# Kernel tuning notes

Measured on AMD Instinct MI355X. Metric: run time of the kernel, lower is better.

Reference implementation:

```python
import jax, jax.numpy as jnp
import numpy as np

B, S, D, H, E, TOPK = 8, 1024, 512, 2048, 8, 2


def setup_inputs() -> dict:
    key = jax.random.key(0)
    ks = jax.random.split(key, 7)
    scale = 0.02
    return {
        "x": jax.random.normal(ks[0], (B, S, D), jnp.float32),
        "gate_w": jax.random.normal(ks[1], (D, E), jnp.float32) * scale,
        "gate_b": jnp.zeros((E,), jnp.float32),
        "w1": jax.random.normal(ks[2], (E, D, H), jnp.float32) * scale,
        "b1": jnp.zeros((E, H), jnp.float32),
        "w2": jax.random.normal(ks[3], (E, H, D), jnp.float32) * scale,
        "b2": jnp.zeros((E, D), jnp.float32),
    }


def reference(x, gate_w, gate_b, w1, b1, w2, b2):
    # ---- MoE transformer MLP (fastmoe FMoETransformerMLP, NaiveGate) ----
    xt = x.reshape(-1, D)                       # [T, D], T = B*S tokens
    logits = xt @ gate_w + gate_b               # [T, E]
    top_val, top_idx = jax.lax.top_k(logits, TOPK)  # [T, k]
    score = jax.nn.softmax(top_val, axis=-1)    # softmax over the k selected logits

    y = jnp.zeros_like(xt)
    # Loop over the small fixed expert set; each token's combine weight for
    # expert e is the sum of its top-k scores routed to e (0 if not selected).
    for e in range(E):
        w_tok = jnp.sum(score * (top_idx == e), axis=-1)        # [T]
        h = jax.nn.gelu(xt @ w1[e] + b1[e], approximate=False)  # [T, H]
        y = y + w_tok[:, None] * (h @ w2[e] + b2[e])            # [T, D]

    y = y.reshape(B, S, D)
    # Outer model: log_softmax over seq of channel-summed features
    return jax.nn.log_softmax(jnp.sum(y, axis=2), axis=1)       # [B, S]
```

## Files before the change

kernel.cpp:

```cpp
#include <hip/hip_runtime.h>
#include <hip/hip_bf16.h>
#include <math.h>

#define T_TOK 8192
#define DIM   512
#define NEXP  8
#define HID   2048
#define NBAT  8
#define SEQ   1024

typedef short  short8 __attribute__((ext_vector_type(8)));
typedef float  f32x4  __attribute__((ext_vector_type(4)));

__device__ __forceinline__ unsigned short f2bf(float f) {
    union { float f; unsigned int u; } v; v.f = f;
    unsigned int u = v.u;
    unsigned int r = u + 0x7FFFu + ((u >> 16) & 1u);
    return (unsigned short)(r >> 16);
}

__device__ __forceinline__ float gelu_f(float v) {
    float v2 = v * v;
    float w = v * (-2.302344f - 0.102955f * v2);
    return v / (1.f + __builtin_amdgcn_exp2f(w));
}

__global__ void prep_k(const float* __restrict__ w1, unsigned short* __restrict__ w1t,
                       const float* __restrict__ w2, const float* __restrict__ b2,
                       float* __restrict__ w2sum, float* __restrict__ b2sum,
                       int* __restrict__ counts) {
    int bid = blockIdx.x;
    int tid = threadIdx.x;
    int wave = tid >> 6, lane = tid & 63;
    if (bid < 2048) {
        __shared__ unsigned short tile[64][65];
        int e = bid >> 8, r = bid & 255;
        int d0 = (r & 7) * 64, h0 = (r >> 3) * 64;
        const float* src = w1 + (size_t)e * DIM * HID;
        #pragma unroll
        for (int pass = 0; pass < 4; ++pass) {
            int dr = pass * 16 + (tid >> 4);
            int hc = (tid & 15) * 4;
            float4 v = *(const float4*)(src + (size_t)(d0 + dr) * HID + h0 + hc);
            tile[hc + 0][dr] = f2bf(v.x);
            tile[hc + 1][dr] = f2bf(v.y);
            tile[hc + 2][dr] = f2bf(v.z);
            tile[hc + 3][dr] = f2bf(v.w);
        }
        __syncthreads();
        unsigned short* dst = w1t + (size_t)e * HID * DIM;
        #pragma unroll
        for (int pass = 0; pass < 4; ++pass) {
            int hr = pass * 16 + (tid >> 4);
            int dc = (tid & 15) * 4;
            ushort4 o;
            o.x = tile[hr][dc];     o.y = tile[hr][dc + 1];
            o.z = tile[hr][dc + 2]; o.w = tile[hr][dc + 3];
            *(ushort4*)(dst + (size_t)(h0 + hr) * DIM + d0 + dc) = o;
        }
    } else if (bid < 2048 + 4096) {
        int row = (bid - 2048) * 4 + wave;
        const float* p = w2 + (size_t)row * DIM;
        float4 a = *(const float4*)(p + lane * 4);
        float4 b = *(const float4*)(p + 256 + lane * 4);
        float s = a.x + a.y + a.z + a.w + b.x + b.y + b.z + b.w;
        #pragma unroll
        for (int off = 32; off >= 1; off >>= 1) s += __shfl_xor(s, off);
        if (lane == 0) w2sum[row] = s;
    } else {
        if (tid < 8) counts[tid] = 0;
        for (int r = wave; r < NEXP; r += 4) {
            const float* p = b2 + (size_t)r * DIM;
            float s = 0.f;
            for (int i = lane; i < DIM; i += 64) s += p[i];
            #pragma unroll
            for (int off = 32; off >= 1; off >>= 1) s += __shfl_xor(s, off);
            if (lane == 0) b2sum[r] = s;
        }
    }
}

__global__ void gate2_k(const float* __restrict__ x, const float* __restrict__ gw,
                        const float* __restrict__ gb, const float* __restrict__ b2sum,
                        unsigned short* __restrict__ xb,
                        int* __restrict__ eidx, float* __restrict__ esc0,
                        float* __restrict__ esc1, float* __restrict__ s_partial) {
    int wave = threadIdx.x >> 6, lane = threadIdx.x & 63;
    int t = blockIdx.x * 4 + wave;
    const float* xp = x + (size_t)t * DIM;
    unsigned short* xbp = xb + (size_t)t * DIM;
    float acc[8] = {0, 0, 0, 0, 0, 0, 0, 0};
    #pragma unroll
    for (int it = 0; it < 8; ++it) {
        int d = it * 64 + lane;
        float xv = xp[d];
        xbp[d] = f2bf(xv);
        float4 g0 = *(const float4*)(gw + d * 8);
        float4 g1 = *(const float4*)(gw + d * 8 + 4);
        acc[0] += xv * g0.x; acc[1] += xv * g0.y; acc[2] += xv * g0.z; acc[3] += xv * g0.w;
        acc[4] += xv * g1.x; acc[5] += xv * g1.y; acc[6] += xv * g1.z; acc[7] += xv * g1.w;
    }
    #pragma unroll
    for (int e = 0; e < 8; ++e) {
        float s = acc[e];
        #pragma unroll
        for (int off = 32; off >= 1; off >>= 1) s += __shfl_xor(s, off);
        acc[e] = s + gb[e];
    }
    float v0 = -1e30f, v1 = -1e30f; int i0 = 0, i1 = 0;
    #pragma unroll
    for (int e = 0; e < 8; ++e) {
        float v = acc[e];
        if (v > v0) { v1 = v0; i1 = i0; v0 = v; i0 = e; }
        else if (v > v1) { v1 = v; i1 = e; }
    }
    float e1 = expf(v1 - v0);
    float inv = 1.f / (1.f + e1);
    float s0 = inv, s1 = e1 * inv;
    if (lane == 0) {
        eidx[t] = i0 | (i1 << 4);
        esc0[t] = s0;
        esc1[t] = s1;
        s_partial[t] = s0 * b2sum[i0] + s1 * b2sum[i1];
    }
}

__global__ __launch_bounds__(1024) void route_k(
    const int* __restrict__ eidx, const float* __restrict__ esc0,
    const float* __restrict__ esc1, int* __restrict__ counts,
    int* __restrict__ ptok, float* __restrict__ pscore) {
    int tid = threadIdx.x;
    int t = blockIdx.x * 1024 + tid;
    int wv = tid >> 6, lane = tid & 63;
    int pk = eidx[t];
    int i0 = pk & 0xf, i1 = (pk >> 4) & 0xf;
    float s0 = esc0[t], s1 = esc1[t];

    __shared__ int waveCnt[16][8];
    __shared__ int waveBase[16][8];

    unsigned long long m0[8], m1[8];
    #pragma unroll
    for (int e = 0; e < 8; ++e) {
        m0[e] = __ballot(i0 == e);
        m1[e] = __ballot(i1 == e);
    }
    if (lane < 8) {
        int c = 0;
        #pragma unroll
        for (int e = 0; e < 8; ++e)
            if (lane == e) c = __popcll(m0[e]) + __popcll(m1[e]);
        waveCnt[wv][lane] = c;
    }
    __syncthreads();
    if (tid < 8) {
        int e = tid;
        int total = 0;
        #pragma unroll
        for (int w = 0; w < 16; ++w) total += waveCnt[w][e];
        int base = atomicAdd(&counts[e], total);
        int run = base;
        #pragma unroll
        for (int w = 0; w < 16; ++w) {
            waveBase[w][e] = run;
            run += waveCnt[w][e];
        }
    }
    __syncthreads();

    unsigned long long lt = (1ULL << lane) - 1ULL;
    int slot0 = 0, slot1 = 0;
    #pragma unroll
    for (int e = 0; e < 8; ++e) {
        if (i0 == e) slot0 = waveBase[wv][e] + __popcll(m0[e] & lt);
        if (i1 == e) slot1 = waveBase[wv][e] + __popcll(m0[e]) + __popcll(m1[e] & lt);
    }
    ptok[i0 * T_TOK + slot0] = t;  pscore[i0 * T_TOK + slot0] = s0;
    ptok[i1 * T_TOK + slot1] = t;  pscore[i1 * T_TOK + slot1] = s1;
}

#define GPTR(p) (const __attribute__((address_space(1))) void*)(p)
#define LPTR(p) (__attribute__((address_space(3))) void*)(p)

__global__ __launch_bounds__(256) void moe_gemm_k(
    const unsigned short* __restrict__ xb, const unsigned short* __restrict__ w1t,
    const float* __restrict__ b1, const float* __restrict__ w2sum,
    const int* __restrict__ counts, const int* __restrict__ ptok,
    const float* __restrict__ pscore, float* __restrict__ s_partial) {

    int bx = blockIdx.x;
    int e = 8, rowBase = 0, accT = 0;
    #pragma unroll
    for (int i = 0; i < 8; ++i) {
        int nt = (counts[i] + 127) >> 7;
        if (e == 8 && bx < accT + nt) { e = i; rowBase = (bx - accT) * 128; }
        accT += nt;
    }
    if (e == 8) return;
    int n_e = counts[e];
    int hBase = blockIdx.y * 128;

    __shared__ unsigned short A_s[128 * 64];
    __shared__ unsigned short B_s[128 * 64];
    __shared__ int   tokLds[128];
    __shared__ float scoreLds[128];

    int tid = threadIdx.x;
    int wave = tid >> 6, lane = tid & 63;

    if (tid < 128) {
        int r = rowBase + tid;
        bool valid = r < n_e;
        tokLds[tid]   = valid ? ptok[e * T_TOK + r]   : 0;
        scoreLds[tid] = valid ? pscore[e * T_TOK + r] : 0.f;
    }
    __syncthreads();

    const unsigned short* gA[4];
    const unsigned short* gB[4];
    int lo[4];
    #pragma unroll
    for (int i = 0; i < 4; ++i) {
        int c = (i * 4 + wave) * 64 + lane;
        int row = c >> 3, pos = c & 7;
        int j = (pos ^ (row & 7)) * 8;
        gA[i] = xb + (size_t)tokLds[row] * DIM + j;
        gB[i] = w1t + ((size_t)e * HID + hBase + row) * DIM + j;
        lo[i] = c * 8;
    }

    int wm = wave >> 1, wn = wave & 1;
    int quad = lane >> 4, col = lane & 15;

    f32x4 acc[4][4];
    #pragma unroll
    for (int m = 0; m < 4; ++m)
        #pragma unroll
        for (int n = 0; n < 4; ++n)
            acc[m][n] = (f32x4){0.f, 0.f, 0.f, 0.f};

    for (int kk = 0; kk < 8; ++kk) {
        __syncthreads();
        int ko = kk * 64;
        #pragma unroll
        for (int i = 0; i < 4; ++i) {
            __builtin_amdgcn_global_load_lds(GPTR(gA[i] + ko), LPTR(&A_s[lo[i]]), 16, 0, 0);
            __builtin_amdgcn_global_load_lds(GPTR(gB[i] + ko), LPTR(&B_s[lo[i]]), 16, 0, 0);
        }
        __syncthreads();
        #pragma unroll
        for (int kh = 0; kh < 2; ++kh) {
            int swz = (((kh << 2) | quad) ^ (col & 7)) * 8;
            const unsigned short* aB = A_s + (wm * 64 + col) * 64 + swz;
            const unsigned short* bB = B_s + (wn * 64 + col) * 64 + swz;
            short8 af[4], bf[4];
            #pragma unroll
            for (int m = 0; m < 4; ++m) af[m] = *(const short8*)(aB + m * 16 * 64);
            #pragma unroll
            for (int n = 0; n < 4; ++n) bf[n] = *(const short8*)(bB + n * 16 * 64);
            #pragma unroll
            for (int m = 0; m < 4; ++m)
                #pragma unroll
                for (int n = 0; n < 4; ++n)
                    acc[m][n] = __builtin_amdgcn_mfma_f32_16x16x32_bf16(af[m], bf[n], acc[m][n], 0, 0, 0);
        }
    }

    const float* b1e = b1 + e * HID;
    const float* w2e = w2sum + e * HID;
    float bias[4], wsum[4];
    #pragma unroll
    for (int n = 0; n < 4; ++n) {
        int h = hBase + wn * 64 + n * 16 + col;
        bias[n] = b1e[h];
        wsum[n] = w2e[h];
    }
    #pragma unroll
    for (int m = 0; m < 4; ++m) {
        float rp0 = 0.f, rp1 = 0.f, rp2 = 0.f, rp3 = 0.f;
        #pragma unroll
        for (int n = 0; n < 4; ++n) {
            rp0 += gelu_f(acc[m][n][0] + bias[n]) * wsum[n];
            rp1 += gelu_f(acc[m][n][1] + bias[n]) * wsum[n];
            rp2 += gelu_f(acc[m][n][2] + bias[n]) * wsum[n];
            rp3 += gelu_f(acc[m][n][3] + bias[n]) * wsum[n];
        }
        #pragma unroll
        for (int off = 8; off >= 1; off >>= 1) {
            rp0 += __shfl_xor(rp0, off);
            rp1 += __shfl_xor(rp1, off);
            rp2 += __shfl_xor(rp2, off);
            rp3 += __shfl_xor(rp3, off);
        }
        if (col < 4) {
            float mine = (col == 0) ? rp0 : (col == 1) ? rp1 : (col == 2) ? rp2 : rp3;
            int rl = wm * 64 + m * 16 + quad * 4 + col;
            int r = rowBase + rl;
            if (r < n_e)
                atomicAdd(&s_partial[tokLds[rl]], scoreLds[rl] * mine);
        }
    }
}

__global__ void lsm_k(const float* __restrict__ s, float* __restrict__ out) {
    int b = blockIdx.x, tid = threadIdx.x;
    int wave = tid >> 6, lane = tid & 63;
    __shared__ float red[4];
    const float* sp = s + (size_t)b * SEQ;
    float v[4];
    #pragma unroll
    for (int i = 0; i < 4; ++i) v[i] = sp[tid + i * 256];
    float m = fmaxf(fmaxf(v[0], v[1]), fmaxf(v[2], v[3]));
    #pragma unroll
    for (int off = 32; off >= 1; off >>= 1) m = fmaxf(m, __shfl_xor(m, off));
    if (lane == 0) red[wave] = m;
    __syncthreads();
    m = fmaxf(fmaxf(red[0], red[1]), fmaxf(red[2], red[3]));
    __syncthreads();
    float t = 0.f;
    #pragma unroll
    for (int i = 0; i < 4; ++i) t += expf(v[i] - m);
    #pragma unroll
    for (int off = 32; off >= 1; off >>= 1) t += __shfl_xor(t, off);
    if (lane == 0) red[wave] = t;
    __syncthreads();
    t = red[0] + red[1] + red[2] + red[3];
    float L = m + logf(t);
    #pragma unroll
    for (int i = 0; i < 4; ++i) out[(size_t)b * SEQ + tid + i * 256] = v[i] - L;
}

extern "C" void kernel_launch(void* const* d_in, const int* in_sizes, int n_in,
                              void* d_out, int out_size, void* d_ws, size_t ws_size,
                              hipStream_t stream) {
    const float* x  = (const float*)d_in[0];
    const float* gw = (const float*)d_in[1];
    const float* gb = (const float*)d_in[2];
    const float* w1 = (const float*)d_in[3];
    const float* b1 = (const float*)d_in[4];
    const float* w2 = (const float*)d_in[5];
    const float* b2 = (const float*)d_in[6];
    float* out = (float*)d_out;

    char* ws = (char*)d_ws;
    int*   counts    = (int*)  (ws + 0);
    float* b2sum     = (float*)(ws + 1280);
    float* s_partial = (float*)(ws + 1536);
    float* w2sum     = (float*)(ws + 34304);
    int*   ptok      = (int*)  (ws + 99840);
    float* pscore    = (float*)(ws + 361984);
    int*   eidx      = (int*)  (ws + 624128);
    float* esc0      = (float*)(ws + 656896);
    float* esc1      = (float*)(ws + 689664);
    unsigned short* xb  = (unsigned short*)(ws + 722432);
    unsigned short* w1t = (unsigned short*)(ws + 9111040);

    prep_k<<<2048 + 4096 + 1, 256, 0, stream>>>(w1, w1t, w2, b2, w2sum, b2sum, counts);
    gate2_k<<<T_TOK / 4, 256, 0, stream>>>(x, gw, gb, b2sum, xb, eidx, esc0, esc1, s_partial);
    route_k<<<NEXP, 1024, 0, stream>>>(eidx, esc0, esc1, counts, ptok, pscore);
    moe_gemm_k<<<dim3(135, 16), 256, 0, stream>>>(xb, w1t, b1, w2sum, counts, ptok, pscore, s_partial);
    lsm_k<<<NBAT, 256, 0, stream>>>(s_partial, out);
}
```

Measured before the change: 214.7 us.

## Double-buffer GEMM LDS tiles and fuse gate into prep kernel

The expert GEMM kernel now uses two LDS buffers, prefetching two K-steps ahead with global_load_lds and explicit vmcnt waits, so global loads overlap MFMA work. It also raises wave priority around the MFMA block. Separately, the gate/top-k kernel is merged into the weight-prep launch, and the s_partial bias term moves to route_k, which saves one kernel launch. The trade-off is double the LDS use, which may lower occupancy, and hand-written waitcnt counts that must match the number of outstanding loads.

```diff
diff --git a/kernel.cpp b/kernel.cpp
--- a/kernel.cpp
+++ b/kernel.cpp
@@ -25,10 +25,15 @@
     return v / (1.f + __builtin_amdgcn_exp2f(w));
 }
 
-__global__ void prep_k(const float* __restrict__ w1, unsigned short* __restrict__ w1t,
-                       const float* __restrict__ w2, const float* __restrict__ b2,
-                       float* __restrict__ w2sum, float* __restrict__ b2sum,
-                       int* __restrict__ counts) {
+__global__ void prep_gate_k(const float* __restrict__ w1, unsigned short* __restrict__ w1t,
+                            const float* __restrict__ w2, const float* __restrict__ b2,
+                            float* __restrict__ w2sum, float* __restrict__ b2sum,
+                            int* __restrict__ counts,
+                            const float* __restrict__ x, const float* __restrict__ gw,
+                            const float* __restrict__ gb,
+                            unsigned short* __restrict__ xb,
+                            int* __restrict__ eidx, float* __restrict__ esc0,
+                            float* __restrict__ esc1) {
     int bid = blockIdx.x;
     int tid = threadIdx.x;
     int wave = tid >> 6, lane = tid & 63;
@@ -58,8 +63,44 @@
             o.z = tile[hr][dc + 2]; o.w = tile[hr][dc + 3];
             *(ushort4*)(dst + (size_t)(h0 + hr) * DIM + d0 + dc) = o;
         }
-    } else if (bid < 2048 + 4096) {
-        int row = (bid - 2048) * 4 + wave;
+    } else if (bid < 4096) {
+        int t = (bid - 2048) * 4 + wave;
+        const float* xp = x + (size_t)t * DIM;
+        unsigned short* xbp = xb + (size_t)t * DIM;
+        float acc[8] = {0, 0, 0, 0, 0, 0, 0, 0};
+        #pragma unroll
+        for (int it = 0; it < 8; ++it) {
+            int d = it * 64 + lane;
+            float xv = xp[d];
+            xbp[d] = f2bf(xv);
+            float4 g0 = *(const float4*)(gw + d * 8);
+            float4 g1 = *(const float4*)(gw + d * 8 + 4);
+            acc[0] += xv * g0.x; acc[1] += xv * g0.y; acc[2] += xv * g0.z; acc[3] += xv * g0.w;
+            acc[4] += xv * g1.x; acc[5] += xv * g1.y; acc[6] += xv * g1.z; acc[7] += xv * g1.w;
+        }
+        #pragma unroll
+        for (int e = 0; e < 8; ++e) {
+            float s = acc[e];
+            #pragma unroll
+            for (int off = 32; off >= 1; off >>= 1) s += __shfl_xor(s, off);
+            acc[e] = s + gb[e];
+        }
+        float v0 = -1e30f, v1 = -1e30f; int i0 = 0, i1 = 0;
+        #pragma unroll
+        for (int e = 0; e < 8; ++e) {
+            float v = acc[e];
+            if (v > v0) { v1 = v0; i1 = i0; v0 = v; i0 = e; }
+            else if (v > v1) { v1 = v; i1 = e; }
+        }
+        float e1 = expf(v1 - v0);
+        float inv = 1.f / (1.f + e1);
+        if (lane == 0) {
+            eidx[t] = i0 | (i1 << 4);
+            esc0[t] = inv;
+            esc1[t] = e1 * inv;
+        }
+    } else if (bid < 8192) {
+        int row = (bid - 4096) * 4 + wave;
         const float* p = w2 + (size_t)row * DIM;
         float4 a = *(const float4*)(p + lane * 4);
         float4 b = *(const float4*)(p + 256 + lane * 4);
@@ -80,55 +121,12 @@
     }
 }
 
-__global__ void gate2_k(const float* __restrict__ x, const float* __restrict__ gw,
-                        const float* __restrict__ gb, const float* __restrict__ b2sum,
-                        unsigned short* __restrict__ xb,
-                        int* __restrict__ eidx, float* __restrict__ esc0,
-                        float* __restrict__ esc1, float* __restrict__ s_partial) {
-    int wave = threadIdx.x >> 6, lane = threadIdx.x & 63;
-    int t = blockIdx.x * 4 + wave;
-    const float* xp = x + (size_t)t * DIM;
-    unsigned short* xbp = xb + (size_t)t * DIM;
-    float acc[8] = {0, 0, 0, 0, 0, 0, 0, 0};
-    #pragma unroll
-    for (int it = 0; it < 8; ++it) {
-        int d = it * 64 + lane;
-        float xv = xp[d];
-        xbp[d] = f2bf(xv);
-        float4 g0 = *(const float4*)(gw + d * 8);
-        float4 g1 = *(const float4*)(gw + d * 8 + 4);
-        acc[0] += xv * g0.x; acc[1] += xv * g0.y; acc[2] += xv * g0.z; acc[3] += xv * g0.w;
-        acc[4] += xv * g1.x; acc[5] += xv * g1.y; acc[6] += xv * g1.z; acc[7] += xv * g1.w;
-    }
-    #pragma unroll
-    for (int e = 0; e < 8; ++e) {
-        float s = acc[e];
-        #pragma unroll
-        for (int off = 32; off >= 1; off >>= 1) s += __shfl_xor(s, off);
-        acc[e] = s + gb[e];
-    }
-    float v0 = -1e30f, v1 = -1e30f; int i0 = 0, i1 = 0;
-    #pragma unroll
-    for (int e = 0; e < 8; ++e) {
-        float v = acc[e];
-        if (v > v0) { v1 = v0; i1 = i0; v0 = v; i0 = e; }
-        else if (v > v1) { v1 = v; i1 = e; }
-    }
-    float e1 = expf(v1 - v0);
-    float inv = 1.f / (1.f + e1);
-    float s0 = inv, s1 = e1 * inv;
-    if (lane == 0) {
-        eidx[t] = i0 | (i1 << 4);
-        esc0[t] = s0;
-        esc1[t] = s1;
-        s_partial[t] = s0 * b2sum[i0] + s1 * b2sum[i1];
-    }
-}
-
 __global__ __launch_bounds__(1024) void route_k(
     const int* __restrict__ eidx, const float* __restrict__ esc0,
-    const float* __restrict__ esc1, int* __restrict__ counts,
-    int* __restrict__ ptok, float* __restrict__ pscore) {
+    const float* __restrict__ esc1, const float* __restrict__ b2sum,
+    int* __restrict__ counts,
+    int* __restrict__ ptok, float* __restrict__ pscore,
+    float* __restrict__ s_partial) {
     int tid = threadIdx.x;
     int t = blockIdx.x * 1024 + tid;
     int wv = tid >> 6, lane = tid & 63;
@@ -136,6 +134,8 @@
     int i0 = pk & 0xf, i1 = (pk >> 4) & 0xf;
     float s0 = esc0[t], s1 = esc1[t];
 
+    s_partial[t] = s0 * b2sum[i0] + s1 * b2sum[i1];
+
     __shared__ int waveCnt[16][8];
     __shared__ int waveBase[16][8];
 
@@ -200,8 +200,8 @@
     int n_e = counts[e];
     int hBase = blockIdx.y * 128;
 
-    __shared__ unsigned short A_s[128 * 64];
-    __shared__ unsigned short B_s[128 * 64];
+    __shared__ unsigned short A_s[2][128 * 64];
+    __shared__ unsigned short B_s[2][128 * 64];
     __shared__ int   tokLds[128];
     __shared__ float scoreLds[128];
 
@@ -239,31 +239,57 @@
         for (int n = 0; n < 4; ++n)
             acc[m][n] = (f32x4){0.f, 0.f, 0.f, 0.f};
 
+    #pragma unroll
+    for (int i = 0; i < 4; ++i) {
+        __builtin_amdgcn_global_load_lds(GPTR(gA[i]), LPTR(&A_s[0][lo[i]]), 16, 0, 0);
+        __builtin_amdgcn_global_load_lds(GPTR(gB[i]), LPTR(&B_s[0][lo[i]]), 16, 0, 0);
+    }
+    #pragma unroll
+    for (int i = 0; i < 4; ++i) {
+        __builtin_amdgcn_global_load_lds(GPTR(gA[i] + 64), LPTR(&A_s[1][lo[i]]), 16, 0, 0);
+        __builtin_amdgcn_global_load_lds(GPTR(gB[i] + 64), LPTR(&B_s[1][lo[i]]), 16, 0, 0);
+    }
+
+    #pragma unroll
     for (int kk = 0; kk < 8; ++kk) {
-        __syncthreads();
-        int ko = kk * 64;
-        #pragma unroll
-        for (int i = 0; i < 4; ++i) {
-            __builtin_amdgcn_global_load_lds(GPTR(gA[i] + ko), LPTR(&A_s[lo[i]]), 16, 0, 0);
-            __builtin_amdgcn_global_load_lds(GPTR(gB[i] + ko), LPTR(&B_s[lo[i]]), 16, 0, 0);
-        }
-        __syncthreads();
+        const int cur = kk & 1;
+        if (kk < 7) { asm volatile("s_waitcnt vmcnt(8)" ::: "memory"); }
+        else        { asm volatile("s_waitcnt vmcnt(0)" ::: "memory"); }
+        __builtin_amdgcn_s_barrier();
+
+        short8 af[2][4], bf[2][4];
         #pragma unroll
         for (int kh = 0; kh < 2; ++kh) {
             int swz = (((kh << 2) | quad) ^ (col & 7)) * 8;
-            const unsigned short* aB = A_s + (wm * 64 + col) * 64 + swz;
-            const unsigned short* bB = B_s + (wn * 64 + col) * 64 + swz;
-            short8 af[4], bf[4];
-            #pragma unroll
-            for (int m = 0; m < 4; ++m) af[m] = *(const short8*)(aB + m * 16 * 64);
-            #pragma unroll
-            for (int n = 0; n < 4; ++n) bf[n] = *(const short8*)(bB + n * 16 * 64);
+            const unsigned short* aB = &A_s[cur][(wm * 64 + col) * 64 + swz];
+            const unsigned short* bB = &B_s[cur][(wn * 64 + col) * 64 + swz];
+            #pragma unroll
+            for (int m = 0; m < 4; ++m) af[kh][m] = *(const short8*)(aB + m * 16 * 64);
+            #pragma unroll
+            for (int n = 0; n < 4; ++n) bf[kh][n] = *(const short8*)(bB + n * 16 * 64);
+        }
+        asm volatile("s_waitcnt lgkmcnt(0)" ::: "memory");
+        __builtin_amdgcn_s_barrier();
+
+        if (kk < 6) {
+            int ko = (kk + 2) * 64;
+            #pragma unroll
+            for (int i = 0; i < 4; ++i) {
+                __builtin_amdgcn_global_load_lds(GPTR(gA[i] + ko), LPTR(&A_s[cur][lo[i]]), 16, 0, 0);
+                __builtin_amdgcn_global_load_lds(GPTR(gB[i] + ko), LPTR(&B_s[cur][lo[i]]), 16, 0, 0);
+            }
+        }
+        __builtin_amdgcn_sched_barrier(0);
+
+        __builtin_amdgcn_s_setprio(1);
+        #pragma unroll
+        for (int kh = 0; kh < 2; ++kh)
             #pragma unroll
             for (int m = 0; m < 4; ++m)
                 #pragma unroll
                 for (int n = 0; n < 4; ++n)
-                    acc[m][n] = __builtin_amdgcn_mfma_f32_16x16x32_bf16(af[m], bf[n], acc[m][n], 0, 0, 0);
-        }
+                    acc[m][n] = __builtin_amdgcn_mfma_f32_16x16x32_bf16(af[kh][m], bf[kh][n], acc[m][n], 0, 0, 0);
+        __builtin_amdgcn_s_setprio(0);
     }
 
     const float* b1e = b1 + e * HID;
@@ -355,9 +381,9 @@
     unsigned short* xb  = (unsigned short*)(ws + 722432);
     unsigned short* w1t = (unsigned short*)(ws + 9111040);
 
-    prep_k<<<2048 + 4096 + 1, 256, 0, stream>>>(w1, w1t, w2, b2, w2sum, b2sum, counts);
-    gate2_k<<<T_TOK / 4, 256, 0, stream>>>(x, gw, gb, b2sum, xb, eidx, esc0, esc1, s_partial);
-    route_k<<<NEXP, 1024, 0, stream>>>(eidx, esc0, esc1, counts, ptok, pscore);
+    prep_gate_k<<<8193, 256, 0, stream>>>(w1, w1t, w2, b2, w2sum, b2sum, counts,
+                                          x, gw, gb, xb, eidx, esc0, esc1);
+    route_k<<<NEXP, 1024, 0, stream>>>(eidx, esc0, esc1, b2sum, counts, ptok, pscore, s_partial);
     moe_gemm_k<<<dim3(135, 16), 256, 0, stream>>>(xb, w1t, b1, w2sum, counts, ptok, pscore, s_partial);
     lsm_k<<<NBAT, 256, 0, stream>>>(s_partial, out);
 }
```

Result: faster. 203.0 us (-5.5%).
